# Kernel optimization log

Measured on AMD Instinct MI355X. Metric: run time of the kernel, lower is better.

The kernel has to match this reference:

```python
import jax, jax.numpy as jnp
import numpy as np

B, D, H, A, T = 2048, 512, 512, 18, 16
W_SCALE = 1e-3


def setup_inputs() -> dict:
    key = jax.random.key(0)
    ks = jax.random.split(key, 7)
    xs = jax.random.normal(ks[0], (B, D), dtype=jnp.float32)
    task_id = jax.random.randint(ks[1], (B,), 0, T)
    action = jax.random.randint(ks[2], (B,), 0, A)
    W1 = jax.random.normal(ks[3], (T, D, H), dtype=jnp.float32) * W_SCALE
    b1 = jnp.zeros((T, H), dtype=jnp.float32)
    W2 = jax.random.normal(ks[4], (T, H, A), dtype=jnp.float32) * W_SCALE
    b2 = jnp.zeros((T, A), dtype=jnp.float32)
    return {"xs": xs, "W1": W1, "b1": b1, "W2": W2, "b2": b2,
            "task_id": task_id, "action": action}


def reference(xs, W1, b1, W2, b2, task_id, action):
    # MultiLinear fc1: gather per-sample weight by task_id, batched matmul
    h = jnp.einsum('bd,bdh->bh', xs, W1[task_id]) + b1[task_id]   # [B, H]
    h = jax.nn.relu(h)
    # MultiLinear fc2 -> logits
    logits = jnp.einsum('bh,bha->ba', h, W2[task_id]) + b2[task_id]  # [B, A]
    # Categorical log_prob / entropy
    logp = jax.nn.log_softmax(logits, axis=-1)                       # [B, A]
    log_pi_a = jnp.take_along_axis(logp, action[:, None], axis=-1)   # [B, 1]
    ent = -jnp.sum(jnp.exp(logp) * logp, axis=-1, keepdims=True)     # [B, 1]
    return action, log_pi_a, ent
```

## Files before the change

### kernel.cpp

```cpp
#include <hip/hip_runtime.h>
#include <math.h>

#define B_ 2048
#define D_ 512
#define H_ 512
#define A_ 18
#define T_ 16
#define MTF 16
#define MAXTILESF 144

typedef __attribute__((ext_vector_type(8))) short short8;
typedef __attribute__((ext_vector_type(4))) float f32x4;

#define XSB_OFF  (1 << 20)
#define W2T_OFF  (3 << 20)
#define W1T_OFF  (4 << 20)
#define WS_NEED  (12 << 20)

__device__ __forceinline__ unsigned short f2bf(float f) {
    union { float f; unsigned int u; } v; v.f = f;
    unsigned int u = v.u;
    return (unsigned short)((u + 0x7fffu + ((u >> 16) & 1u)) >> 16);
}

__global__ __launch_bounds__(256) void nk_prep(const float* __restrict__ W1,
                                               const float* __restrict__ xs,
                                               const float* __restrict__ W2,
                                               const int* __restrict__ task_id,
                                               unsigned short* __restrict__ w1t,
                                               unsigned short* __restrict__ xs_b,
                                               unsigned short* __restrict__ w2t,
                                               int* __restrict__ wsi) {
    int bid = blockIdx.x;
    int tid = threadIdx.x;
    if (bid < 1024) {
        __shared__ float tile[64][65];
        int hx = bid & 7, dy = (bid >> 3) & 7, t = bid >> 6;
        int cx = tid & 63, ry = tid >> 6;
        const float* src = W1 + ((size_t)t * D_ + dy * 64) * H_ + hx * 64;
#pragma unroll
        for (int i = 0; i < 16; ++i) {
            int row = i * 4 + ry;
            tile[row][cx] = src[(size_t)row * H_ + cx];
        }
        __syncthreads();
        unsigned short* dst = w1t + ((size_t)t * H_ + hx * 64) * D_ + dy * 64;
        int c4 = tid & 15, hr0 = tid >> 4;
#pragma unroll
        for (int i = 0; i < 4; ++i) {
            int hr = hr0 + i * 16;
            unsigned short uu[4] = { f2bf(tile[c4 * 4 + 0][hr]), f2bf(tile[c4 * 4 + 1][hr]),
                                     f2bf(tile[c4 * 4 + 2][hr]), f2bf(tile[c4 * 4 + 3][hr]) };
            *(uint2*)(dst + (size_t)hr * D_ + c4 * 4) = *(const uint2*)uu;
        }
    } else if (bid < 1536) {
        size_t off = ((size_t)(bid - 1024) * 256 + tid) * 8;
        float4 x0 = *(const float4*)(xs + off);
        float4 x1 = *(const float4*)(xs + off + 4);
        unsigned short uu[8] = { f2bf(x0.x), f2bf(x0.y), f2bf(x0.z), f2bf(x0.w),
                                 f2bf(x1.x), f2bf(x1.y), f2bf(x1.z), f2bf(x1.w) };
        *(uint4*)(xs_b + off) = *(const uint4*)uu;
    } else if (bid < 1552) {
        int t = bid - 1536;
        const float* src = W2 + (size_t)t * H_ * A_;
        unsigned short* dst = w2t + (size_t)t * 32 * H_;
#pragma unroll
        for (int i = 0; i < 2; ++i) {
            int h = tid * 2 + i;
            float v[A_];
#pragma unroll
            for (int a = 0; a < A_; ++a) v[a] = src[(size_t)h * A_ + a];
#pragma unroll
            for (int a = 0; a < A_; ++a) dst[(size_t)a * H_ + h] = f2bf(v[a]);
#pragma unroll
            for (int a = A_; a < 32; ++a) dst[(size_t)a * H_ + h] = 0;
        }
    } else {
        __shared__ int cnt[T_], cur[T_], soff[T_];
        if (tid < T_) { cnt[tid] = 0; cur[tid] = 0; }
        __syncthreads();
        for (int b = tid; b < B_; b += 256) atomicAdd(&cnt[task_id[b]], 1);
        __syncthreads();
        if (tid == 0) {
            int off = 0;
            for (int t = 0; t < T_; ++t) {
                soff[t] = off; wsi[17 + t] = off;
                off += cnt[t];
            }
            wsi[17 + T_] = off;
        }
        __syncthreads();
        for (int b = tid; b < B_; b += 256) {
            int t = task_id[b];
            int pos = atomicAdd(&cur[t], 1);
            wsi[256 + soff[t] + pos] = b;
        }
    }
}

__global__ __launch_bounds__(512) void nk_fused(
        const unsigned short* __restrict__ xs_b,
        const unsigned short* __restrict__ w1t,
        const unsigned short* __restrict__ w2t,
        const float* __restrict__ b1, const float* __restrict__ b2,
        const int* __restrict__ action, float* __restrict__ out,
        const int* __restrict__ wsi) {
    __shared__ unsigned short h_lds[16][520];
    __shared__ float lg_lds[16][34];
    __shared__ int sidx[16];

    int t = blockIdx.x, kt = blockIdx.y;
    int off0 = wsi[17 + t], off1 = wsi[18 + t];
    int rowbase = off0 + kt * 16;
    int rows = off1 - rowbase;
    if (rows <= 0) return;
    if (rows > 16) rows = 16;

    int tid = threadIdx.x, lane = tid & 63, w = tid >> 6;
    int r15 = lane & 15, kg = lane >> 4;

    if (tid < 16) sidx[tid] = wsi[256 + rowbase + (tid < rows ? tid : rows - 1)];
    __syncthreads();

    const unsigned short* ap = xs_b + (size_t)sidx[r15] * D_ + kg * 8;
    const unsigned short* bbase = w1t + (size_t)t * H_ * D_ + kg * 8;
    const unsigned short* bp0 = bbase + (size_t)(w * 64 + r15) * D_;
    const unsigned short* bp1 = bp0 + (size_t)16 * D_;
    const unsigned short* bp2 = bp0 + (size_t)32 * D_;
    const unsigned short* bp3 = bp0 + (size_t)48 * D_;

    f32x4 acc0 = {0.f,0.f,0.f,0.f}, acc1 = {0.f,0.f,0.f,0.f};
    f32x4 acc2 = {0.f,0.f,0.f,0.f}, acc3 = {0.f,0.f,0.f,0.f};
#pragma unroll
    for (int ks = 0; ks < 16; ++ks) {
        short8 af = *(const short8*)(ap + ks * 32);
        short8 b0 = *(const short8*)(bp0 + ks * 32);
        short8 b1f = *(const short8*)(bp1 + ks * 32);
        short8 b2f = *(const short8*)(bp2 + ks * 32);
        short8 b3f = *(const short8*)(bp3 + ks * 32);
        acc0 = __builtin_amdgcn_mfma_f32_16x16x32_bf16(af, b0, acc0, 0, 0, 0);
        acc1 = __builtin_amdgcn_mfma_f32_16x16x32_bf16(af, b1f, acc1, 0, 0, 0);
        acc2 = __builtin_amdgcn_mfma_f32_16x16x32_bf16(af, b2f, acc2, 0, 0, 0);
        acc3 = __builtin_amdgcn_mfma_f32_16x16x32_bf16(af, b3f, acc3, 0, 0, 0);
    }

    int colb = w * 64 + r15;
    float bv0 = b1[t * H_ + colb];
    float bv1 = b1[t * H_ + colb + 16];
    float bv2 = b1[t * H_ + colb + 32];
    float bv3 = b1[t * H_ + colb + 48];
#pragma unroll
    for (int j = 0; j < 4; ++j) {
        int row = kg * 4 + j;
        float v;
        v = acc0[j] + bv0; h_lds[row][colb]      = f2bf(v > 0.f ? v : 0.f);
        v = acc1[j] + bv1; h_lds[row][colb + 16] = f2bf(v > 0.f ? v : 0.f);
        v = acc2[j] + bv2; h_lds[row][colb + 32] = f2bf(v > 0.f ? v : 0.f);
        v = acc3[j] + bv3; h_lds[row][colb + 48] = f2bf(v > 0.f ? v : 0.f);
    }
    __syncthreads();

    if (w == 0) {
        const unsigned short* wa0 = w2t + (size_t)t * 32 * H_ + (size_t)r15 * H_ + kg * 8;
        const unsigned short* wa1 = wa0 + (size_t)16 * H_;
        f32x4 c0 = {0.f,0.f,0.f,0.f}, c1 = {0.f,0.f,0.f,0.f};
#pragma unroll
        for (int ks = 0; ks < 16; ++ks) {
            short8 hf = *(const short8*)&h_lds[r15][ks * 32 + kg * 8];
            short8 w0 = *(const short8*)(wa0 + ks * 32);
            short8 w1f = *(const short8*)(wa1 + ks * 32);
            c0 = __builtin_amdgcn_mfma_f32_16x16x32_bf16(hf, w0, c0, 0, 0, 0);
            c1 = __builtin_amdgcn_mfma_f32_16x16x32_bf16(hf, w1f, c1, 0, 0, 0);
        }
        float bb0 = (r15 < A_) ? b2[t * A_ + r15] : 0.f;
        float bb1 = (16 + r15 < A_) ? b2[t * A_ + 16 + r15] : 0.f;
#pragma unroll
        for (int j = 0; j < 4; ++j) {
            int row = kg * 4 + j;
            lg_lds[row][r15] = c0[j] + bb0;
            lg_lds[row][16 + r15] = c1[j] + bb1;
        }
    }
    __syncthreads();

    if (tid < rows) {
        int b = sidx[tid];
        float logits[A_];
        float m = -1e30f;
#pragma unroll
        for (int a = 0; a < A_; ++a) {
            logits[a] = lg_lds[tid][a];
            m = fmaxf(m, logits[a]);
        }
        float S = 0.f, sle = 0.f;
#pragma unroll
        for (int a = 0; a < A_; ++a) {
            float e = expf(logits[a] - m);
            S += e;
            sle += logits[a] * e;
        }
        float logZ = m + logf(S);
        int as = action[b];
        out[b] = (float)as;
        out[B_ + b] = logits[as] - logZ;
        out[2 * B_ + b] = logZ - sle / S;
    }
}


__global__ void nk_init(int* wsi) { int i = threadIdx.x; if (i < 50) wsi[i] = 0; }

__global__ void nk_count(const int* task_id, int* wsi) {
    int b = blockIdx.x * blockDim.x + threadIdx.x;
    if (b < B_) atomicAdd(&wsi[1 + task_id[b]], 1);
}

__global__ void nk_plan(int* wsi) {
    int off = 0, tot = 0;
    for (int t = 0; t < T_; ++t) {
        wsi[17 + t] = off;
        int cnt = wsi[1 + t];
        int nt = (cnt + MTF - 1) / MTF;
        for (int k = 0; k < nt; ++k) wsi[50 + tot++] = (t << 16) | k;
        off += cnt;
    }
    wsi[17 + T_] = off;
    wsi[0] = tot;
}

__global__ void nk_scatter(const int* task_id, int* wsi) {
    int b = blockIdx.x * blockDim.x + threadIdx.x;
    if (b < B_) {
        int t = task_id[b];
        int pos = atomicAdd(&wsi[34 + t], 1);
        wsi[256 + wsi[17 + t] + pos] = b;
    }
}

__global__ __launch_bounds__(512) void nk_main(
        const float* __restrict__ xs, const float* __restrict__ W1,
        const float* __restrict__ b1, const float* __restrict__ W2,
        const float* __restrict__ b2, const int* __restrict__ task_id,
        const int* __restrict__ action, float* __restrict__ out,
        const int* __restrict__ wsi) {
    __shared__ float tile[MTF][D_];
    __shared__ int sidx[MTF];
    int bid = blockIdx.x;
    if (bid >= wsi[0]) return;
    int code = wsi[50 + bid];
    int t = code >> 16, kt = code & 0xffff;
    int off0 = wsi[17 + t], off1 = wsi[17 + t + 1];
    int base = off0 + kt * MTF;
    int rows = off1 - base; if (rows > MTF) rows = MTF;
    int tid = threadIdx.x;
    if (tid < MTF) sidx[tid] = (tid < rows) ? wsi[256 + base + tid] : -1;
    __syncthreads();
    for (int i = 0; i < MTF; ++i) {
        int b = sidx[i];
        tile[i][tid] = (b >= 0) ? xs[(size_t)b * D_ + tid] : 0.f;
    }
    __syncthreads();
    const float* w1p = W1 + (size_t)t * D_ * H_ + tid;
    float acc[MTF];
#pragma unroll
    for (int i = 0; i < MTF; ++i) acc[i] = 0.f;
    for (int d = 0; d < D_; d += 4) {
        float w0 = w1p[(size_t)(d + 0) * H_];
        float w1v = w1p[(size_t)(d + 1) * H_];
        float w2v = w1p[(size_t)(d + 2) * H_];
        float w3v = w1p[(size_t)(d + 3) * H_];
#pragma unroll
        for (int i = 0; i < MTF; ++i) {
            float4 x = *(const float4*)&tile[i][d];
            float a0 = fmaf(x.x, w0, acc[i]);
            a0 = fmaf(x.y, w1v, a0);
            a0 = fmaf(x.z, w2v, a0);
            acc[i] = fmaf(x.w, w3v, a0);
        }
    }
    __syncthreads();
    float b1v = b1[t * H_ + tid];
#pragma unroll
    for (int i = 0; i < MTF; ++i) {
        float h = acc[i] + b1v;
        tile[i][tid] = h > 0.f ? h : 0.f;
    }
    __syncthreads();
    int g = tid >> 5, l = tid & 31;
    float lg[A_];
#pragma unroll
    for (int a = 0; a < A_; ++a) lg[a] = 0.f;
    const float* w2base = W2 + (size_t)t * H_ * A_;
    for (int hh = l; hh < H_; hh += 32) {
        float hv = tile[g][hh];
        const float* wrow = w2base + (size_t)hh * A_;
#pragma unroll
        for (int a = 0; a < A_; ++a) lg[a] = fmaf(hv, wrow[a], lg[a]);
    }
#pragma unroll
    for (int a = 0; a < A_; ++a) {
        lg[a] += __shfl_down(lg[a], 16, 32);
        lg[a] += __shfl_down(lg[a], 8, 32);
        lg[a] += __shfl_down(lg[a], 4, 32);
        lg[a] += __shfl_down(lg[a], 2, 32);
        lg[a] += __shfl_down(lg[a], 1, 32);
    }
    if (l == 0 && g < rows) {
        int b = sidx[g];
        float logits[A_];
        float m = -1e30f;
#pragma unroll
        for (int a = 0; a < A_; ++a) {
            logits[a] = lg[a] + b2[t * A_ + a];
            m = fmaxf(m, logits[a]);
        }
        float S = 0.f, sle = 0.f;
#pragma unroll
        for (int a = 0; a < A_; ++a) {
            float e = expf(logits[a] - m);
            S += e;
            sle += logits[a] * e;
        }
        float logZ = m + logf(S);
        int as = action[b];
        out[b] = (float)as;
        out[B_ + b] = logits[as] - logZ;
        out[2 * B_ + b] = logZ - sle / S;
    }
}

extern "C" void kernel_launch(void* const* d_in, const int* in_sizes, int n_in,
                              void* d_out, int out_size, void* d_ws, size_t ws_size,
                              hipStream_t stream) {
    const float* xs = (const float*)d_in[0];
    const float* W1 = (const float*)d_in[1];
    const float* b1 = (const float*)d_in[2];
    const float* W2 = (const float*)d_in[3];
    const float* b2 = (const float*)d_in[4];
    const int* task_id = (const int*)d_in[5];
    const int* action = (const int*)d_in[6];
    float* out = (float*)d_out;

    if (ws_size >= WS_NEED) {
        unsigned char* wsb = (unsigned char*)d_ws;
        int* wsi = (int*)d_ws;
        unsigned short* xs_b = (unsigned short*)(wsb + XSB_OFF);
        unsigned short* w2t = (unsigned short*)(wsb + W2T_OFF);
        unsigned short* w1t = (unsigned short*)(wsb + W1T_OFF);

        nk_prep<<<1553, 256, 0, stream>>>(W1, xs, W2, task_id, w1t, xs_b, w2t, wsi);
        nk_fused<<<dim3(T_, 128), 512, 0, stream>>>(xs_b, w1t, w2t, b1, b2,
                                                    action, out, wsi);
    } else {
        int* wsi = (int*)d_ws;
        nk_init<<<1, 64, 0, stream>>>(wsi);
        nk_count<<<(B_ + 255) / 256, 256, 0, stream>>>(task_id, wsi);
        nk_plan<<<1, 1, 0, stream>>>(wsi);
        nk_scatter<<<(B_ + 255) / 256, 256, 0, stream>>>(task_id, wsi);
        nk_main<<<MAXTILESF, 512, 0, stream>>>(xs, W1, b1, W2, b2, task_id, action, out, wsi);
    }
}
```

Before: 35.67 us.

## Fuse xs bf16 conversion into main kernel and use persistent task-pair tiling

The separate xs-to-bf16 conversion blocks in the prep kernel are removed. The fused kernel now loads the gathered fp32 rows of xs, converts them to bf16 and stages them in LDS. The fused grid changes from T×128 mostly-empty blocks to 8×NSLOT blocks, each looping over the tiles of two tasks, and the fc2 MFMA work is split across two waves. This removes a prep pass and its workspace traffic and avoids launching many blocks that exit immediately. In exchange, each block runs its tiles serially and adds extra barriers.

```diff
diff --git a/kernel.cpp b/kernel.cpp
--- a/kernel.cpp
+++ b/kernel.cpp
@@ -8,11 +8,11 @@
 #define T_ 16
 #define MTF 16
 #define MAXTILESF 144
+#define NSLOT 24
 
 typedef __attribute__((ext_vector_type(8))) short short8;
 typedef __attribute__((ext_vector_type(4))) float f32x4;
 
-#define XSB_OFF  (1 << 20)
 #define W2T_OFF  (3 << 20)
 #define W1T_OFF  (4 << 20)
 #define WS_NEED  (12 << 20)
@@ -24,11 +24,9 @@
 }
 
 __global__ __launch_bounds__(256) void nk_prep(const float* __restrict__ W1,
-                                               const float* __restrict__ xs,
                                                const float* __restrict__ W2,
                                                const int* __restrict__ task_id,
                                                unsigned short* __restrict__ w1t,
-                                               unsigned short* __restrict__ xs_b,
                                                unsigned short* __restrict__ w2t,
                                                int* __restrict__ wsi) {
     int bid = blockIdx.x;
@@ -53,15 +51,8 @@
                                      f2bf(tile[c4 * 4 + 2][hr]), f2bf(tile[c4 * 4 + 3][hr]) };
             *(uint2*)(dst + (size_t)hr * D_ + c4 * 4) = *(const uint2*)uu;
         }
-    } else if (bid < 1536) {
-        size_t off = ((size_t)(bid - 1024) * 256 + tid) * 8;
-        float4 x0 = *(const float4*)(xs + off);
-        float4 x1 = *(const float4*)(xs + off + 4);
-        unsigned short uu[8] = { f2bf(x0.x), f2bf(x0.y), f2bf(x0.z), f2bf(x0.w),
-                                 f2bf(x1.x), f2bf(x1.y), f2bf(x1.z), f2bf(x1.w) };
-        *(uint4*)(xs_b + off) = *(const uint4*)uu;
-    } else if (bid < 1552) {
-        int t = bid - 1536;
+    } else if (bid < 1040) {
+        int t = bid - 1024;
         const float* src = W2 + (size_t)t * H_ * A_;
         unsigned short* dst = w2t + (size_t)t * 32 * H_;
 #pragma unroll
@@ -99,111 +90,132 @@
 }
 
 __global__ __launch_bounds__(512) void nk_fused(
-        const unsigned short* __restrict__ xs_b,
+        const float* __restrict__ xs,
         const unsigned short* __restrict__ w1t,
         const unsigned short* __restrict__ w2t,
         const float* __restrict__ b1, const float* __restrict__ b2,
         const int* __restrict__ action, float* __restrict__ out,
         const int* __restrict__ wsi) {
+    __shared__ unsigned short x_lds[16][520];
     __shared__ unsigned short h_lds[16][520];
     __shared__ float lg_lds[16][34];
     __shared__ int sidx[16];
 
-    int t = blockIdx.x, kt = blockIdx.y;
-    int off0 = wsi[17 + t], off1 = wsi[18 + t];
-    int rowbase = off0 + kt * 16;
-    int rows = off1 - rowbase;
-    if (rows <= 0) return;
-    if (rows > 16) rows = 16;
-
+    int c = blockIdx.x;
     int tid = threadIdx.x, lane = tid & 63, w = tid >> 6;
     int r15 = lane & 15, kg = lane >> 4;
 
-    if (tid < 16) sidx[tid] = wsi[256 + rowbase + (tid < rows ? tid : rows - 1)];
-    __syncthreads();
-
-    const unsigned short* ap = xs_b + (size_t)sidx[r15] * D_ + kg * 8;
-    const unsigned short* bbase = w1t + (size_t)t * H_ * D_ + kg * 8;
-    const unsigned short* bp0 = bbase + (size_t)(w * 64 + r15) * D_;
-    const unsigned short* bp1 = bp0 + (size_t)16 * D_;
-    const unsigned short* bp2 = bp0 + (size_t)32 * D_;
-    const unsigned short* bp3 = bp0 + (size_t)48 * D_;
-
-    f32x4 acc0 = {0.f,0.f,0.f,0.f}, acc1 = {0.f,0.f,0.f,0.f};
-    f32x4 acc2 = {0.f,0.f,0.f,0.f}, acc3 = {0.f,0.f,0.f,0.f};
-#pragma unroll
-    for (int ks = 0; ks < 16; ++ks) {
-        short8 af = *(const short8*)(ap + ks * 32);
-        short8 b0 = *(const short8*)(bp0 + ks * 32);
-        short8 b1f = *(const short8*)(bp1 + ks * 32);
-        short8 b2f = *(const short8*)(bp2 + ks * 32);
-        short8 b3f = *(const short8*)(bp3 + ks * 32);
-        acc0 = __builtin_amdgcn_mfma_f32_16x16x32_bf16(af, b0, acc0, 0, 0, 0);
-        acc1 = __builtin_amdgcn_mfma_f32_16x16x32_bf16(af, b1f, acc1, 0, 0, 0);
-        acc2 = __builtin_amdgcn_mfma_f32_16x16x32_bf16(af, b2f, acc2, 0, 0, 0);
-        acc3 = __builtin_amdgcn_mfma_f32_16x16x32_bf16(af, b3f, acc3, 0, 0, 0);
-    }
-
-    int colb = w * 64 + r15;
-    float bv0 = b1[t * H_ + colb];
-    float bv1 = b1[t * H_ + colb + 16];
-    float bv2 = b1[t * H_ + colb + 32];
-    float bv3 = b1[t * H_ + colb + 48];
-#pragma unroll
-    for (int j = 0; j < 4; ++j) {
-        int row = kg * 4 + j;
-        float v;
-        v = acc0[j] + bv0; h_lds[row][colb]      = f2bf(v > 0.f ? v : 0.f);
-        v = acc1[j] + bv1; h_lds[row][colb + 16] = f2bf(v > 0.f ? v : 0.f);
-        v = acc2[j] + bv2; h_lds[row][colb + 32] = f2bf(v > 0.f ? v : 0.f);
-        v = acc3[j] + bv3; h_lds[row][colb + 48] = f2bf(v > 0.f ? v : 0.f);
-    }
-    __syncthreads();
-
-    if (w == 0) {
-        const unsigned short* wa0 = w2t + (size_t)t * 32 * H_ + (size_t)r15 * H_ + kg * 8;
-        const unsigned short* wa1 = wa0 + (size_t)16 * H_;
-        f32x4 c0 = {0.f,0.f,0.f,0.f}, c1 = {0.f,0.f,0.f,0.f};
+    int o0 = wsi[17 + c],     n0 = wsi[18 + c] - o0;
+    int o1 = wsi[17 + c + 8], n1 = wsi[18 + c + 8] - o1;
+    int nt0 = (n0 + 15) >> 4, nt1 = (n1 + 15) >> 4;
+    int ntot = nt0 + nt1;
+
+    for (int u = blockIdx.y; u < ntot; u += NSLOT) {
+        int t, kt, off0, rT;
+        if (u < nt0) { t = c; kt = u; off0 = o0; rT = n0; }
+        else { t = c + 8; kt = u - nt0; off0 = o1; rT = n1; }
+        int rowbase = off0 + kt * 16;
+        int rows = rT - kt * 16; if (rows > 16) rows = 16;
+
+        if (tid < 16) sidx[tid] = wsi[256 + rowbase + (tid < rows ? tid : rows - 1)];
+        __syncthreads();
+
+        {
+            int row = tid >> 5, col = (tid & 31) * 16;
+            const float* src = xs + (size_t)sidx[row] * D_ + col;
+            float4 v0 = *(const float4*)(src);
+            float4 v1 = *(const float4*)(src + 4);
+            float4 v2 = *(const float4*)(src + 8);
+            float4 v3 = *(const float4*)(src + 12);
+            unsigned short uu[16] = {
+                f2bf(v0.x), f2bf(v0.y), f2bf(v0.z), f2bf(v0.w),
+                f2bf(v1.x), f2bf(v1.y), f2bf(v1.z), f2bf(v1.w),
+                f2bf(v2.x), f2bf(v2.y), f2bf(v2.z), f2bf(v2.w),
+                f2bf(v3.x), f2bf(v3.y), f2bf(v3.z), f2bf(v3.w) };
+            *(uint4*)&x_lds[row][col]     = *(const uint4*)&uu[0];
+            *(uint4*)&x_lds[row][col + 8] = *(const uint4*)&uu[8];
+        }
+        __syncthreads();
+
+        const unsigned short* bbase = w1t + (size_t)t * H_ * D_ + kg * 8;
+        const unsigned short* bp0 = bbase + (size_t)(w * 64 + r15) * D_;
+        const unsigned short* bp1 = bp0 + (size_t)16 * D_;
+        const unsigned short* bp2 = bp0 + (size_t)32 * D_;
+        const unsigned short* bp3 = bp0 + (size_t)48 * D_;
+
+        f32x4 acc0 = {0.f,0.f,0.f,0.f}, acc1 = {0.f,0.f,0.f,0.f};
+        f32x4 acc2 = {0.f,0.f,0.f,0.f}, acc3 = {0.f,0.f,0.f,0.f};
 #pragma unroll
         for (int ks = 0; ks < 16; ++ks) {
-            short8 hf = *(const short8*)&h_lds[r15][ks * 32 + kg * 8];
-            short8 w0 = *(const short8*)(wa0 + ks * 32);
-            short8 w1f = *(const short8*)(wa1 + ks * 32);
-            c0 = __builtin_amdgcn_mfma_f32_16x16x32_bf16(hf, w0, c0, 0, 0, 0);
-            c1 = __builtin_amdgcn_mfma_f32_16x16x32_bf16(hf, w1f, c1, 0, 0, 0);
-        }
-        float bb0 = (r15 < A_) ? b2[t * A_ + r15] : 0.f;
-        float bb1 = (16 + r15 < A_) ? b2[t * A_ + 16 + r15] : 0.f;
+            short8 af = *(const short8*)&x_lds[r15][ks * 32 + kg * 8];
+            short8 b0 = *(const short8*)(bp0 + ks * 32);
+            short8 b1f = *(const short8*)(bp1 + ks * 32);
+            short8 b2f = *(const short8*)(bp2 + ks * 32);
+            short8 b3f = *(const short8*)(bp3 + ks * 32);
+            acc0 = __builtin_amdgcn_mfma_f32_16x16x32_bf16(af, b0, acc0, 0, 0, 0);
+            acc1 = __builtin_amdgcn_mfma_f32_16x16x32_bf16(af, b1f, acc1, 0, 0, 0);
+            acc2 = __builtin_amdgcn_mfma_f32_16x16x32_bf16(af, b2f, acc2, 0, 0, 0);
+            acc3 = __builtin_amdgcn_mfma_f32_16x16x32_bf16(af, b3f, acc3, 0, 0, 0);
+        }
+
+        int colb = w * 64 + r15;
+        float bv0 = b1[t * H_ + colb];
+        float bv1 = b1[t * H_ + colb + 16];
+        float bv2 = b1[t * H_ + colb + 32];
+        float bv3 = b1[t * H_ + colb + 48];
 #pragma unroll
         for (int j = 0; j < 4; ++j) {
             int row = kg * 4 + j;
-            lg_lds[row][r15] = c0[j] + bb0;
-            lg_lds[row][16 + r15] = c1[j] + bb1;
-        }
-    }
-    __syncthreads();
-
-    if (tid < rows) {
-        int b = sidx[tid];
-        float logits[A_];
-        float m = -1e30f;
-#pragma unroll
-        for (int a = 0; a < A_; ++a) {
-            logits[a] = lg_lds[tid][a];
-            m = fmaxf(m, logits[a]);
-        }
-        float S = 0.f, sle = 0.f;
-#pragma unroll
-        for (int a = 0; a < A_; ++a) {
-            float e = expf(logits[a] - m);
-            S += e;
-            sle += logits[a] * e;
-        }
-        float logZ = m + logf(S);
-        int as = action[b];
-        out[b] = (float)as;
-        out[B_ + b] = logits[as] - logZ;
-        out[2 * B_ + b] = logZ - sle / S;
+            float v;
+            v = acc0[j] + bv0; h_lds[row][colb]      = f2bf(v > 0.f ? v : 0.f);
+            v = acc1[j] + bv1; h_lds[row][colb + 16] = f2bf(v > 0.f ? v : 0.f);
+            v = acc2[j] + bv2; h_lds[row][colb + 32] = f2bf(v > 0.f ? v : 0.f);
+            v = acc3[j] + bv3; h_lds[row][colb + 48] = f2bf(v > 0.f ? v : 0.f);
+        }
+        __syncthreads();
+
+        if (w < 2) {
+            const unsigned short* wa = w2t + (size_t)t * 32 * H_
+                                       + (size_t)(w * 16 + r15) * H_ + kg * 8;
+            f32x4 c0 = {0.f,0.f,0.f,0.f};
+#pragma unroll
+            for (int ks = 0; ks < 16; ++ks) {
+                short8 hf = *(const short8*)&h_lds[r15][ks * 32 + kg * 8];
+                short8 w0 = *(const short8*)(wa + ks * 32);
+                c0 = __builtin_amdgcn_mfma_f32_16x16x32_bf16(hf, w0, c0, 0, 0, 0);
+            }
+            int a = w * 16 + r15;
+            float bb = (a < A_) ? b2[t * A_ + a] : 0.f;
+#pragma unroll
+            for (int j = 0; j < 4; ++j) {
+                lg_lds[kg * 4 + j][a] = c0[j] + bb;
+            }
+        }
+        __syncthreads();
+
+        if (tid < rows) {
+            int b = sidx[tid];
+            float logits[A_];
+            float m = -1e30f;
+#pragma unroll
+            for (int a = 0; a < A_; ++a) {
+                logits[a] = lg_lds[tid][a];
+                m = fmaxf(m, logits[a]);
+            }
+            float S = 0.f, sle = 0.f;
+#pragma unroll
+            for (int a = 0; a < A_; ++a) {
+                float e = expf(logits[a] - m);
+                S += e;
+                sle += logits[a] * e;
+            }
+            float logZ = m + logf(S);
+            int as = action[b];
+            out[b] = (float)as;
+            out[B_ + b] = logits[as] - logZ;
+            out[2 * B_ + b] = logZ - sle / S;
+        }
+        __syncthreads();
     }
 }
 
@@ -344,13 +356,12 @@
     if (ws_size >= WS_NEED) {
         unsigned char* wsb = (unsigned char*)d_ws;
         int* wsi = (int*)d_ws;
-        unsigned short* xs_b = (unsigned short*)(wsb + XSB_OFF);
         unsigned short* w2t = (unsigned short*)(wsb + W2T_OFF);
         unsigned short* w1t = (unsigned short*)(wsb + W1T_OFF);
 
-        nk_prep<<<1553, 256, 0, stream>>>(W1, xs, W2, task_id, w1t, xs_b, w2t, wsi);
-        nk_fused<<<dim3(T_, 128), 512, 0, stream>>>(xs_b, w1t, w2t, b1, b2,
-                                                    action, out, wsi);
+        nk_prep<<<1041, 256, 0, stream>>>(W1, W2, task_id, w1t, w2t, wsi);
+        nk_fused<<<dim3(8, NSLOT), 512, 0, stream>>>(xs, w1t, w2t, b1, b2,
+                                                     action, out, wsi);
     } else {
         int* wsi = (int*)d_ws;
         nk_init<<<1, 64, 0, stream>>>(wsi);
```

Result: faster. 31.40 us (-12.0%).
